# Optimization experiments

Hardware: AMD Instinct MI355X
Metric: run time of the kernel (lower is better)

Reference implementation:

```python
import jax, jax.numpy as jnp
import numpy as np

B, S, D = 2, 1024, 4096
N_HEADS, KV_HEADS, HEAD_DIM = 32, 8, 128
EPS = 1e-6
ROPE_THETA = 1e6


def setup_inputs() -> dict:
    key = jax.random.key(0)
    ks = jax.random.split(key, 7)
    scale = 0.02
    x = jax.random.normal(ks[0], (B, S, D), dtype=jnp.float32)
    positions = jnp.broadcast_to(jnp.arange(S, dtype=jnp.int32)[None, :], (B, S))
    wq = jax.random.normal(ks[1], (D, N_HEADS, HEAD_DIM), dtype=jnp.float32) * scale
    wk = jax.random.normal(ks[2], (D, KV_HEADS, HEAD_DIM), dtype=jnp.float32) * scale
    wv = jax.random.normal(ks[3], (D, KV_HEADS, HEAD_DIM), dtype=jnp.float32) * scale
    wo = jax.random.normal(ks[4], (N_HEADS, HEAD_DIM, D), dtype=jnp.float32) * scale
    q_norm_w = 1.0 + jax.random.normal(ks[5], (HEAD_DIM,), dtype=jnp.float32) * 0.01
    k_norm_w = 1.0 + jax.random.normal(ks[6], (HEAD_DIM,), dtype=jnp.float32) * 0.01
    return {"x": x, "positions": positions, "wq": wq, "wk": wk, "wv": wv,
            "wo": wo, "q_norm_w": q_norm_w, "k_norm_w": k_norm_w}


def _rms_norm(t, w):
    # per-head RMSNorm over last (head_dim) axis
    var = jnp.mean(jnp.square(t), axis=-1, keepdims=True)
    return (t * jax.lax.rsqrt(var + EPS)) * w


def _rope(t, positions):
    # neox-style rotary embedding; t: [B, S, n, H], positions: [B, S]
    half = t.shape[-1] // 2
    inv_freq = 1.0 / (ROPE_THETA ** (jnp.arange(0, half, dtype=jnp.float32) / half))
    ang = positions.astype(jnp.float32)[..., None] * inv_freq  # [B, S, half]
    cos = jnp.cos(ang)[:, :, None, :]  # [B, S, 1, half]
    sin = jnp.sin(ang)[:, :, None, :]
    t1, t2 = t[..., :half], t[..., half:]
    return jnp.concatenate([t1 * cos - t2 * sin, t2 * cos + t1 * sin], axis=-1)


def reference(x, positions, wq, wk, wv, wo, q_norm_w, k_norm_w):
    # QKV projections (einsum layers: 'bsd,dnh->bsnh')
    q = jnp.einsum('bsd,dnh->bsnh', x, wq)  # [B, S, N, H]
    k = jnp.einsum('bsd,dkh->bskh', x, wk)  # [B, S, K, H]
    v = jnp.einsum('bsd,dkh->bskh', x, wv)
    # per-head QK RMSNorm, then RoPE
    q = _rope(_rms_norm(q, q_norm_w), positions)
    k = _rope(_rms_norm(k, k_norm_w), positions)
    # GQA: expand KV heads to query heads
    groups = N_HEADS // KV_HEADS
    k = jnp.repeat(k, groups, axis=2)  # [B, S, N, H]
    v = jnp.repeat(v, groups, axis=2)
    sm_scale = HEAD_DIM ** -0.5
    scores = jnp.einsum('bqnh,btnh->bnqt', q, k) * sm_scale  # [B, N, S, S]
    causal = jnp.tril(jnp.ones((S, S), dtype=bool))
    scores = jnp.where(causal[None, None], scores, jnp.finfo(scores.dtype).min)
    probs = jax.nn.softmax(scores, axis=-1)
    attn = jnp.einsum('bnqt,btnh->bqnh', probs, v)  # [B, S, N, H]
    out = jnp.einsum('bqnh,nhd->bqd', attn, wo)  # output projection
    return out
```

## Files before the change

kernel.cpp:

```cpp
#include <hip/hip_runtime.h>
#include <stdint.h>

#define S_LEN   1024
#define D_MODEL 4096
#define NHQ     32
#define NKV     8
#define HD      128
#define NTOK    2048
#define NQKV    6144
#define SM_SCALE 0.08838834764831843f

typedef __attribute__((ext_vector_type(8))) __bf16 bf16x8;
typedef __attribute__((ext_vector_type(4))) float f32x4;

__device__ __forceinline__ unsigned short f2bf(float f) {
  union { float f; unsigned u; } x; x.f = f;
  unsigned r = x.u + 0x7fffu + ((x.u >> 16) & 1u);
  return (unsigned short)(r >> 16);
}

__device__ __forceinline__ void gload_lds16(const void* g, void* l) {
  __builtin_amdgcn_global_load_lds((__attribute__((address_space(1))) void*)g,
                                   (__attribute__((address_space(3))) void*)l,
                                   16, 0, 0);
}

__global__ void k_f32_to_bf16(const float* __restrict__ in,
                              unsigned short* __restrict__ out, int n8) {
  int i = blockIdx.x * blockDim.x + threadIdx.x;
  if (i >= n8) return;
  const float4* p = (const float4*)(in + (size_t)i * 8);
  float4 v0 = p[0], v1 = p[1];
  uint4 o;
  o.x = f2bf(v0.x) | ((unsigned)f2bf(v0.y) << 16);
  o.y = f2bf(v0.z) | ((unsigned)f2bf(v0.w) << 16);
  o.z = f2bf(v1.x) | ((unsigned)f2bf(v1.y) << 16);
  o.w = f2bf(v1.z) | ((unsigned)f2bf(v1.w) << 16);
  *(uint4*)(out + (size_t)i * 8) = o;
}

__global__ void k_transpose(const float* __restrict__ in,
                            unsigned short* __restrict__ out, int R, int C) {
  __shared__ float t[32][33];
  int c = threadIdx.x & 31, r0 = threadIdx.x >> 5;
  int cb = blockIdx.x * 32, rb = blockIdx.y * 32;
#pragma unroll
  for (int i = 0; i < 4; ++i) {
    int r = r0 + i * 8;
    t[r][c] = in[(size_t)(rb + r) * C + cb + c];
  }
  __syncthreads();
#pragma unroll
  for (int i = 0; i < 4; ++i) {
    int r = r0 + i * 8;
    out[(size_t)(cb + r) * R + rb + c] = f2bf(t[c][r]);
  }
}


#define STG(Gptr, rowbase, ksrc, half, bufi, matoff)                            \
  { int kcl = (ksrc) < NT ? (ksrc) : NT - 1;                                    \
    _Pragma("unroll")                                                           \
    for (int i_ = 0; i_ < 2; ++i_) {                                            \
      int lin = i_ * 512 + tid;                                                 \
      int r_ = lin >> 2, slot = lin & 3;                                        \
      int sw = slot ^ ((r_ >> 1) & 3);                                          \
      gload_lds16(Gptr + (size_t)((rowbase) + r_) * Kstride + k0e + kcl * 64 + (half) * 32 + sw * 8, \
                  smem + (bufi) * 65536 + (matoff) + (half) * 16384 + lin * 16); \
    } }

#define RD_AF(dst, mh, ks, bufi)                                                \
  _Pragma("unroll")                                                             \
  for (int mf = 0; mf < 4; ++mf) {                                              \
    int row = wr * 128 + (mh) * 64 + mf * 16 + lr;                              \
    dst[mf] = *(const bf16x8*)(smem + (bufi) * 65536 + (ks) * 16384 + row * 64  \
                               + ((lg * 16) ^ (((row >> 1) & 3) << 4)));        \
  }

#define RD_BF(dst, ks, bufi)                                                    \
  _Pragma("unroll")                                                             \
  for (int nf = 0; nf < 4; ++nf) {                                              \
    int row = wc * 64 + nf * 16 + lr;                                           \
    dst[nf] = *(const bf16x8*)(smem + (bufi) * 65536 + 32768 + (ks) * 16384 + row * 64 \
                               + ((lg * 16) ^ (((row >> 1) & 3) << 4)));        \
  }

#define MFMA16(mh, AF, BF)                                                      \
  __builtin_amdgcn_s_setprio(1);                                                \
  _Pragma("unroll")                                                             \
  for (int mf = 0; mf < 4; ++mf)                                                \
    _Pragma("unroll")                                                           \
    for (int nf = 0; nf < 4; ++nf)                                              \
      acc[(mh) * 4 + mf][nf] = __builtin_amdgcn_mfma_f32_16x16x32_bf16(         \
          AF[mf], BF[nf], acc[(mh) * 4 + mf][nf], 0, 0, 0);                     \
  __builtin_amdgcn_s_setprio(0);

#define PHASE(STG_STMT, RD_STMT, MFMA_STMT)                                     \
  asm volatile("s_waitcnt lgkmcnt(0)" ::: "memory");                            \
  __builtin_amdgcn_sched_barrier(0);                                            \
  STG_STMT;                                                                     \
  asm volatile("s_waitcnt vmcnt(6)" ::: "memory");                              \
  RD_STMT;                                                                      \
  __builtin_amdgcn_sched_barrier(0);                                            \
  MFMA_STMT;                                                                    \
  __builtin_amdgcn_s_barrier();

__global__ __launch_bounds__(512, 2) void k_gemm256(
    const unsigned short* __restrict__ A,
    const unsigned short* __restrict__ Bt,
    float* __restrict__ C, int Kstride, int ldc, int nbx, int ksplit, int NT,
    int use_atomic) {
  extern __shared__ __align__(16) char smem[];
  int tid = threadIdx.x;
  int l = tid & 63;
  int w = tid >> 6;
  int lr = l & 15, lg = l >> 4;
  int wr = w >> 2, wc = w & 3;
  int nwg = gridDim.x;
  int q8 = nwg >> 3;
  int o = blockIdx.x;
  int wg = (o & 7) * q8 + (o >> 3);
  int tiles = nwg / ksplit;
  int ks = wg / tiles;
  int wgt = wg - ks * tiles;
  int by = wgt / nbx, bx = wgt - by * nbx;
  int bm = by * 256, bn = bx * 256;
  int k0e = ks * NT * 64;

  f32x4 acc[8][4] = {};
  bf16x8 af0[4], af1[4], bf0[4], bf1[4];

  STG(A, bm, 0, 0, 0, 0); STG(Bt, bn, 0, 0, 0, 32768);
  STG(A, bm, 0, 1, 0, 0); STG(Bt, bn, 0, 1, 0, 32768);
  STG(A, bm, 1, 0, 1, 0); STG(Bt, bn, 1, 0, 1, 32768);
  asm volatile("s_waitcnt vmcnt(8)" ::: "memory");
  __builtin_amdgcn_s_barrier();
  RD_AF(af0, 0, 0, 0) RD_BF(bf0, 0, 0)

  for (int kt = 0; kt < NT; ++kt) {
    int cur = kt & 1;
    PHASE(STG(A, bm, kt + 1, 1, cur ^ 1, 0),
          { RD_AF(af1, 1, 0, cur) },
          MFMA16(0, af0, bf0))
    PHASE(STG(Bt, bn, kt + 1, 1, cur ^ 1, 32768),
          { RD_AF(af0, 0, 1, cur) RD_BF(bf1, 1, cur) },
          MFMA16(1, af1, bf0))
    PHASE(STG(A, bm, kt + 2, 0, cur, 0),
          { RD_AF(af1, 1, 1, cur) },
          MFMA16(0, af0, bf1))
    PHASE(STG(Bt, bn, kt + 2, 0, cur, 32768),
          { RD_AF(af0, 0, 0, cur ^ 1) RD_BF(bf0, 0, cur ^ 1) },
          MFMA16(1, af1, bf1))
  }

#pragma unroll
  for (int mh = 0; mh < 2; ++mh)
#pragma unroll
    for (int mf = 0; mf < 4; ++mf)
#pragma unroll
      for (int nf = 0; nf < 4; ++nf)
#pragma unroll
        for (int j = 0; j < 4; ++j) {
          size_t idx = (size_t)(bm + wr * 128 + mh * 64 + mf * 16 + lg * 4 + j) * ldc +
                       bn + wc * 64 + nf * 16 + lr;
          float v = acc[mh * 4 + mf][nf][j];
          if (use_atomic) atomicAdd(&C[idx], v);
          else C[idx] = v;
        }
}

__global__ void k_norm_rope(const float* __restrict__ qkv, const float* __restrict__ w,
                            const int* __restrict__ positions,
                            unsigned short* __restrict__ out, int nheads, int colbase,
                            float oscale) {
  int wid = blockIdx.x * 4 + (threadIdx.x >> 6);
  int lane = threadIdx.x & 63;
  int token = wid / nheads, head = wid - token * nheads;
  const float* src = qkv + (size_t)token * NQKV + colbase + head * HD;
  float e0 = src[lane], e1 = src[lane + 64];
  float ss = e0 * e0 + e1 * e1;
#pragma unroll
  for (int m = 1; m < 64; m <<= 1) ss += __shfl_xor(ss, m, 64);
  float rs = rsqrtf(ss * (1.0f / 128.0f) + 1e-6f);
  float n0 = e0 * rs * w[lane], n1 = e1 * rs * w[lane + 64];
  int pos = positions[token];
  float invf = exp2f((float)lane * (-19.931568569324174f / 64.0f));
  float ang = (float)pos * invf;
  float sv, cv;
  sincosf(ang, &sv, &cv);
  float o0 = (n0 * cv - n1 * sv) * oscale;
  float o1 = (n1 * cv + n0 * sv) * oscale;
  int b = token >> 10, s = token & 1023;
  size_t ob = ((size_t)(b * nheads + head) * S_LEN + s) * HD;
  out[ob + lane] = f2bf(o0);
  out[ob + 64 + lane] = f2bf(o1);
}

__global__ void k_v_transpose(const float* __restrict__ qkv, unsigned short* __restrict__ vt) {
  __shared__ float t[32][33];
  int slice = blockIdx.z;
  int b = slice >> 3, kh = slice & 7;
  const float* in = qkv + (size_t)(b * S_LEN) * NQKV + 5120 + kh * HD;
  unsigned short* out = vt + (size_t)slice * HD * S_LEN;
  int c = threadIdx.x & 31, r0 = threadIdx.x >> 5;
  int s0 = blockIdx.y * 32, d0 = blockIdx.x * 32;
#pragma unroll
  for (int i = 0; i < 4; ++i) {
    int r = r0 + i * 8;
    t[r][c] = in[(size_t)(s0 + r) * NQKV + d0 + c];
  }
  __syncthreads();
#pragma unroll
  for (int i = 0; i < 4; ++i) {
    int r = r0 + i * 8;
    out[(size_t)(d0 + r) * S_LEN + s0 + c] = f2bf(t[c][r]);
  }
}

__global__ __launch_bounds__(256) void k_attn(const unsigned short* __restrict__ qh,
                                              const unsigned short* __restrict__ kbuf,
                                              const unsigned short* __restrict__ vtbuf,
                                              unsigned short* __restrict__ attn_out) {
  __shared__ __align__(16) unsigned short k_lds[64 * 128];
  __shared__ __align__(16) unsigned short v_lds[128 * 64];
  __shared__ __align__(16) unsigned short p_lds[4][16 * 64];
  int b = blockIdx.z, h = blockIdx.y, bx = blockIdx.x;
  int khd = h >> 2;
  int tid = threadIdx.x, w = tid >> 6, l = tid & 63;
  int lr = l & 15, lg = l >> 4;
  const unsigned short* K = kbuf + (size_t)(b * NKV + khd) * S_LEN * HD;
  const unsigned short* VT = vtbuf + (size_t)(b * NKV + khd) * HD * S_LEN;
  char* klp = (char*)k_lds;
  char* vlp = (char*)v_lds;
  char* plp = (char*)p_lds[w];
  int swz = (lr & 7) << 4;

  for (int strip = 0; strip < 2; ++strip) {
    int qs = strip ? (15 - bx) : bx;
    int q0 = qs * 64;
    const unsigned short* Q = qh + ((size_t)(b * NHQ + h) * S_LEN + q0 + w * 16) * HD;
    bf16x8 qf[4];
#pragma unroll
    for (int kk = 0; kk < 4; ++kk)
      qf[kk] = *(const bf16x8*)&Q[(size_t)lr * HD + kk * 32 + lg * 8];

    f32x4 o[8] = {};
    float m_[4], l_[4];
#pragma unroll
    for (int j = 0; j < 4; ++j) { m_[j] = -1e30f; l_[j] = 0.0f; }

    int nt = qs + 1;
    for (int t = 0; t < nt; ++t) {
      int t0 = t * 64;
      __syncthreads();
#pragma unroll
      for (int it = 0; it < 4; ++it) {
        int db = (tid + it * 256) * 16;
        int kr = db >> 8, kc = db & 255;
        gload_lds16(K + (size_t)(t0 + kr) * HD + ((kc ^ ((kr & 7) << 4)) >> 1), klp + db);
        int vr = db >> 7, vc = db & 127;
        gload_lds16(VT + (size_t)vr * S_LEN + t0 + ((vc ^ ((vr & 7) << 4)) >> 1), vlp + db);
      }
      __syncthreads();

      f32x4 sc[4];
      __builtin_amdgcn_s_setprio(1);
#pragma unroll
      for (int ct = 0; ct < 4; ++ct) {
        f32x4 s = {};
        int row = ct * 16 + lr;
#pragma unroll
        for (int kk = 0; kk < 4; ++kk) {
          bf16x8 kf = *(const bf16x8*)(klp + row * 256 + ((kk * 64 + lg * 16) ^ swz));
          s = __builtin_amdgcn_mfma_f32_16x16x32_bf16(qf[kk], kf, s, 0, 0, 0);
        }
        sc[ct] = s;
      }
      __builtin_amdgcn_s_setprio(0);

      bool full = (t < qs);
      float alpha[4];
#pragma unroll
      for (int j = 0; j < 4; ++j) {
        if (!full) {
          int rg = q0 + w * 16 + lg * 4 + j;
#pragma unroll
          for (int ct = 0; ct < 4; ++ct)
            sc[ct][j] = (t0 + ct * 16 + lr <= rg) ? sc[ct][j] : -1e30f;
        }
        float mx = fmaxf(fmaxf(sc[0][j], sc[1][j]), fmaxf(sc[2][j], sc[3][j]));
#pragma unroll
        for (int msk = 1; msk < 16; msk <<= 1) mx = fmaxf(mx, __shfl_xor(mx, msk, 64));
        float mn = fmaxf(m_[j], mx);
        alpha[j] = __expf(m_[j] - mn);
        int q = lg * 4 + j;
        int psw = (q & 7) << 4;
        float ps = 0.0f;
#pragma unroll
        for (int ct = 0; ct < 4; ++ct) {
          float p = __expf(sc[ct][j] - mn);
          ps += p;
          *(unsigned short*)(plp + q * 128 + (((ct * 16 + lr) * 2) ^ psw)) = f2bf(p);
        }
#pragma unroll
        for (int msk = 1; msk < 16; msk <<= 1) ps += __shfl_xor(ps, msk, 64);
        l_[j] = l_[j] * alpha[j] + ps;
        m_[j] = mn;
      }
#pragma unroll
      for (int dc = 0; dc < 8; ++dc) {
        o[dc][0] *= alpha[0]; o[dc][1] *= alpha[1];
        o[dc][2] *= alpha[2]; o[dc][3] *= alpha[3];
      }
      asm volatile("s_waitcnt lgkmcnt(0)" ::: "memory");
      __builtin_amdgcn_s_setprio(1);
#pragma unroll
      for (int kt = 0; kt < 2; ++kt) {
        bf16x8 pa = *(const bf16x8*)(plp + lr * 128 + ((kt * 64 + lg * 16) ^ swz));
#pragma unroll
        for (int dc = 0; dc < 8; ++dc) {
          int vrow = dc * 16 + lr;
          bf16x8 vf = *(const bf16x8*)(vlp + vrow * 128 + ((kt * 64 + lg * 16) ^ swz));
          o[dc] = __builtin_amdgcn_mfma_f32_16x16x32_bf16(pa, vf, o[dc], 0, 0, 0);
        }
      }
      __builtin_amdgcn_s_setprio(0);
    }

#pragma unroll
    for (int j = 0; j < 4; ++j) {
      int rg = q0 + w * 16 + lg * 4 + j;
      size_t row = (size_t)(b * S_LEN + rg) * D_MODEL + h * HD;
      float inv = 1.0f / l_[j];
#pragma unroll
      for (int dc = 0; dc < 8; ++dc)
        attn_out[row + dc * 16 + lr] = f2bf(o[dc][j] * inv);
    }
  }
}

extern "C" void kernel_launch(void* const* d_in, const int* in_sizes, int n_in,
                              void* d_out, int out_size, void* d_ws, size_t ws_size,
                              hipStream_t stream) {
  const float* x        = (const float*)d_in[0];
  const int* positions  = (const int*)d_in[1];
  const float* wq       = (const float*)d_in[2];
  const float* wk       = (const float*)d_in[3];
  const float* wv       = (const float*)d_in[4];
  const float* wo       = (const float*)d_in[5];
  const float* qnw      = (const float*)d_in[6];
  const float* knw      = (const float*)d_in[7];
  float* out            = (float*)d_out;

  char* ws = (char*)d_ws;
  unsigned short* xb   = (unsigned short*)(ws);
  unsigned short* wB   = (unsigned short*)(ws + 16777216);
  unsigned short* woT  = (unsigned short*)(ws + 67108864);
  float*          qkv  = (float*)(ws + 100663296);
  unsigned short* qh   = wB;
  unsigned short* khb  = (unsigned short*)(ws + 33554432);
  unsigned short* vtb  = (unsigned short*)(ws + 37748736);
  unsigned short* attn = xb;

  dim3 tb(256);
  hipMemsetAsync(out, 0, (size_t)out_size * 4, stream);

  k_f32_to_bf16<<<4096, tb, 0, stream>>>(x, xb, 1048576);
  k_transpose<<<dim3(128, 128), tb, 0, stream>>>(wq, wB, 4096, 4096);
  k_transpose<<<dim3(32, 128), tb, 0, stream>>>(wk, wB + (size_t)4096 * 4096, 4096, 1024);
  k_transpose<<<dim3(32, 128), tb, 0, stream>>>(wv, wB + (size_t)5120 * 4096, 4096, 1024);
  k_transpose<<<dim3(128, 128), tb, 0, stream>>>(wo, woT, 4096, 4096);

  k_gemm256<<<dim3(192), dim3(512), 131072, stream>>>(xb, wB, qkv, 4096, 6144, 24, 1, 64, 0);

  k_norm_rope<<<16384, tb, 0, stream>>>(qkv, qnw, positions, qh, 32, 0, SM_SCALE);
  k_norm_rope<<<4096, tb, 0, stream>>>(qkv, knw, positions, khb, 8, 4096, 1.0f);
  k_v_transpose<<<dim3(4, 32, 16), tb, 0, stream>>>(qkv, vtb);

  k_attn<<<dim3(8, 32, 2), tb, 0, stream>>>(qh, khb, vtb, attn);

  k_gemm256<<<dim3(256), dim3(512), 131072, stream>>>(attn, woT, out, 4096, 4096, 16, 2, 32, 1);
}
```

Baseline: 372.5 us.

## Restructure GEMM main loop to single-buffered fragments with shallower prefetch

```diff
diff --git a/kernel.cpp b/kernel.cpp
--- a/kernel.cpp
+++ b/kernel.cpp
@@ -69,40 +69,35 @@
                   smem + (bufi) * 65536 + (matoff) + (half) * 16384 + lin * 16); \
     } }
 
-#define RD_AF(dst, mh, ks, bufi)                                                \
+#define RD_A(mh, kh, bufi)                                                      \
   _Pragma("unroll")                                                             \
   for (int mf = 0; mf < 4; ++mf) {                                              \
     int row = wr * 128 + (mh) * 64 + mf * 16 + lr;                              \
-    dst[mf] = *(const bf16x8*)(smem + (bufi) * 65536 + (ks) * 16384 + row * 64  \
-                               + ((lg * 16) ^ (((row >> 1) & 3) << 4)));        \
-  }
-
-#define RD_BF(dst, ks, bufi)                                                    \
+    af[mf] = *(const bf16x8*)(smem + (bufi) * 65536 + (kh) * 16384 + row * 64   \
+                              + ((lg * 16) ^ (((row >> 1) & 3) << 4)));         \
+  }
+
+#define RD_B(kh, bufi)                                                          \
   _Pragma("unroll")                                                             \
   for (int nf = 0; nf < 4; ++nf) {                                              \
     int row = wc * 64 + nf * 16 + lr;                                           \
-    dst[nf] = *(const bf16x8*)(smem + (bufi) * 65536 + 32768 + (ks) * 16384 + row * 64 \
-                               + ((lg * 16) ^ (((row >> 1) & 3) << 4)));        \
-  }
-
-#define MFMA16(mh, AF, BF)                                                      \
+    bf[nf] = *(const bf16x8*)(smem + (bufi) * 65536 + 32768 + (kh) * 16384 + row * 64 \
+                              + ((lg * 16) ^ (((row >> 1) & 3) << 4)));         \
+  }
+
+#define PHASE_TAIL(mh, GATE)                                                    \
+  if (GATE) asm volatile("s_waitcnt vmcnt(4)" ::: "memory");                    \
+  __builtin_amdgcn_s_barrier();                                                 \
+  asm volatile("s_waitcnt lgkmcnt(0)" ::: "memory");                            \
+  __builtin_amdgcn_sched_barrier(0);                                            \
   __builtin_amdgcn_s_setprio(1);                                                \
   _Pragma("unroll")                                                             \
   for (int mf = 0; mf < 4; ++mf)                                                \
     _Pragma("unroll")                                                           \
     for (int nf = 0; nf < 4; ++nf)                                              \
       acc[(mh) * 4 + mf][nf] = __builtin_amdgcn_mfma_f32_16x16x32_bf16(         \
-          AF[mf], BF[nf], acc[(mh) * 4 + mf][nf], 0, 0, 0);                     \
-  __builtin_amdgcn_s_setprio(0);
-
-#define PHASE(STG_STMT, RD_STMT, MFMA_STMT)                                     \
-  asm volatile("s_waitcnt lgkmcnt(0)" ::: "memory");                            \
-  __builtin_amdgcn_sched_barrier(0);                                            \
-  STG_STMT;                                                                     \
-  asm volatile("s_waitcnt vmcnt(6)" ::: "memory");                              \
-  RD_STMT;                                                                      \
-  __builtin_amdgcn_sched_barrier(0);                                            \
-  MFMA_STMT;                                                                    \
+          af[mf], bf[nf], acc[(mh) * 4 + mf][nf], 0, 0, 0);                     \
+  __builtin_amdgcn_s_setprio(0);                                                \
   __builtin_amdgcn_s_barrier();
 
 __global__ __launch_bounds__(512, 2) void k_gemm256(
@@ -128,29 +123,27 @@
   int k0e = ks * NT * 64;
 
   f32x4 acc[8][4] = {};
-  bf16x8 af0[4], af1[4], bf0[4], bf1[4];
+  bf16x8 af[4], bf[4];
 
   STG(A, bm, 0, 0, 0, 0); STG(Bt, bn, 0, 0, 0, 32768);
   STG(A, bm, 0, 1, 0, 0); STG(Bt, bn, 0, 1, 0, 32768);
-  STG(A, bm, 1, 0, 1, 0); STG(Bt, bn, 1, 0, 1, 32768);
-  asm volatile("s_waitcnt vmcnt(8)" ::: "memory");
+  asm volatile("s_waitcnt vmcnt(4)" ::: "memory");
   __builtin_amdgcn_s_barrier();
-  RD_AF(af0, 0, 0, 0) RD_BF(bf0, 0, 0)
 
   for (int kt = 0; kt < NT; ++kt) {
     int cur = kt & 1;
-    PHASE(STG(A, bm, kt + 1, 1, cur ^ 1, 0),
-          { RD_AF(af1, 1, 0, cur) },
-          MFMA16(0, af0, bf0))
-    PHASE(STG(Bt, bn, kt + 1, 1, cur ^ 1, 32768),
-          { RD_AF(af0, 0, 1, cur) RD_BF(bf1, 1, cur) },
-          MFMA16(1, af1, bf0))
-    PHASE(STG(A, bm, kt + 2, 0, cur, 0),
-          { RD_AF(af1, 1, 1, cur) },
-          MFMA16(0, af0, bf1))
-    PHASE(STG(Bt, bn, kt + 2, 0, cur, 32768),
-          { RD_AF(af0, 0, 0, cur ^ 1) RD_BF(bf0, 0, cur ^ 1) },
-          MFMA16(1, af1, bf1))
+    RD_A(0, 0, cur) RD_B(0, cur)
+    STG(A, bm, kt + 1, 0, cur ^ 1, 0)
+    PHASE_TAIL(0, 0)
+    RD_A(1, 0, cur)
+    STG(Bt, bn, kt + 1, 0, cur ^ 1, 32768)
+    PHASE_TAIL(1, 1)
+    RD_A(0, 1, cur) RD_B(1, cur)
+    STG(A, bm, kt + 1, 1, cur ^ 1, 0)
+    PHASE_TAIL(0, 0)
+    RD_A(1, 1, cur)
+    STG(Bt, bn, kt + 1, 1, cur ^ 1, 32768)
+    PHASE_TAIL(1, 1)
   }
 
 #pragma unroll
```

After: 375.4 us. No clear change (+0.8%).
